# Performance work log

Measured on AMD Instinct MI355X. Metric: run time of the kernel, lower is better.

The kernel has to match this reference:

```python
import jax, jax.numpy as jnp
import numpy as np

RRF_K = 60.0
NUM_DOCS = 1_000_000


def setup_inputs() -> dict:
    key = jax.random.key(0)
    k1, k2, k3 = jax.random.split(key, 3)
    B, T, K = 60, 4, 100
    return {
        "index_tensor": jax.random.randint(k1, (B, T, K), 0, NUM_DOCS, dtype=jnp.int64 if jax.config.jax_enable_x64 else jnp.int32).astype(jnp.int32),
        "ranking_tensor": jax.random.uniform(k2, (B, T, K), dtype=jnp.float32),
        "weight": jnp.ones((T,), dtype=jnp.float32),
        "pos_positions": jax.random.randint(k3, (B,), 0, 5, dtype=jnp.int32),
        "num_docs": NUM_DOCS,
    }


def reference(index_tensor, ranking_tensor, weight, pos_positions, num_docs):
    # index_tensor: [B, T, K] doc ids; ranking_tensor: [B, T, K] teacher scores/ranks
    B = index_tensor.shape[0]
    # weighted reciprocal-rank-fusion score per retrieved doc: w_t / (RRF_K + rank)
    rrf = weight[None, :, None] / (RRF_K + ranking_tensor)  # [B, T, K]
    flat_idx = index_tensor.reshape(B, -1)                  # [B, T*K]
    flat_s = rrf.reshape(B, -1)                             # [B, T*K]
    # batched scatter-add into the per-query fused score vector [B, num_docs]
    fused = jnp.zeros((B, num_docs), dtype=ranking_tensor.dtype)
    fused = fused.at[jnp.arange(B)[:, None], flat_idx].add(flat_s)
    # full descending argsort per query (torch.argsort(..., descending=True))
    order = jnp.argsort(-fused, axis=1)                     # [B, num_docs]
    positive_idx = order[jnp.arange(B), pos_positions]      # [B]
    return order, positive_idx
```

## Files before the change

kernel.cpp:

```cpp
#include <hip/hip_runtime.h>
#include <hip/hip_bf16.h>

#define T_DIM 4
#define K_DIM 100
#define NPER 400
#define NDOCS 1000000
#define FILL_BLOCK 256
#define FILL_PER_THREAD 32
#define FILL_CHUNK (FILL_BLOCK * FILL_PER_THREAD)
#define BLOCKS_PER_ROW ((NDOCS + FILL_CHUNK - 1) / FILL_CHUNK)
#define QN (FILL_PER_THREAD / 4)

__global__ __launch_bounds__(512) void rrf_prep_kernel(
    const int* __restrict__ idx, const float* __restrict__ rnk,
    const float* __restrict__ weight, const int* __restrict__ pos,
    int* __restrict__ wsA, int* __restrict__ wsHead, int* __restrict__ wsNnz,
    int* __restrict__ out_pos)
{
  const int b = blockIdx.x;
  const int tid = threadIdx.x;
  const int lane = tid & 63, wave = tid >> 6;

  __shared__ int   ids[NPER];
  __shared__ float sc[NPER];
  __shared__ int   sid[NPER];
  __shared__ float ssc[NPER];
  __shared__ int   uid[NPER];
  __shared__ float usc[NPER];
  __shared__ int   head[NPER];
  __shared__ int   wsum[8];

  if (tid < NPER) {
    ids[tid] = idx[b * NPER + tid];
    sc[tid]  = weight[tid / K_DIM] / (60.0f + rnk[b * NPER + tid]);
  }
  __syncthreads();

  if (tid < NPER) {
    const int myid = ids[tid];
    int r = 0;
    for (int j = 0; j < NPER; ++j) {
      const int oj = ids[j];
      r += (oj < myid) || (oj == myid && j < tid);
    }
    sid[r] = myid;
    ssc[r] = sc[tid];
  }
  __syncthreads();

  int isLeader = 0;
  float mysum = 0.0f;
  if (tid < NPER) {
    isLeader = (tid == 0) || (sid[tid] != sid[tid - 1]);
    if (isLeader) {
      mysum = ssc[tid];
      for (int k = tid + 1; k < NPER && sid[k] == sid[tid]; ++k) mysum += ssc[k];
    }
  }

  int val = isLeader;
#pragma unroll
  for (int off = 1; off < 64; off <<= 1) {
    int n = __shfl_up(val, off, 64);
    if (lane >= off) val += n;
  }
  if (lane == 63) wsum[wave] = val;
  __syncthreads();
  if (wave == 0 && lane < 8) {
    int wv = wsum[lane];
#pragma unroll
    for (int off = 1; off < 8; off <<= 1) {
      int n = __shfl_up(wv, off, 8);
      if ((lane & 7) >= off) wv += n;
    }
    wsum[lane] = wv;
  }
  __syncthreads();
  const int incl = val + (wave > 0 ? wsum[wave - 1] : 0);
  const int nnz  = wsum[7];

  if (isLeader) {
    const int u = incl - 1;
    uid[u] = sid[tid];
    usc[u] = mysum;
  }
  __syncthreads();

  if (tid < nnz) {
    const float si = usc[tid];
    const int   ii = uid[tid];
    int r2 = 0;
    for (int j = 0; j < nnz; ++j) {
      const float sj = usc[j];
      r2 += (sj > si) || (sj == si && uid[j] < ii);
    }
    head[r2] = ii;
  }
  __syncthreads();

  if (tid < nnz) {
    wsA[b * NPER + tid]    = uid[tid] - tid;
    wsHead[b * NPER + tid] = head[tid];
  }
  if (tid == 0) {
    wsNnz[b]   = nnz;
    out_pos[b] = head[pos[b]];
  }
}

__global__ __launch_bounds__(FILL_BLOCK) void rrf_fill_kernel(
    const int* __restrict__ wsA, const int* __restrict__ wsHead,
    const int* __restrict__ wsNnz, int* __restrict__ out)
{
  const int row   = blockIdx.x / BLOCKS_PER_ROW;
  const int chunk = blockIdx.x % BLOCKS_PER_ROW;
  const int tid   = threadIdx.x;

  __shared__ int A[NPER];
  __shared__ int H[NPER];
  __shared__ int s_nnz;

  for (int i = tid; i < NPER; i += FILL_BLOCK)
    A[i] = wsA[row * NPER + i];
  if (chunk == 0)
    for (int i = tid; i < NPER; i += FILL_BLOCK)
      H[i] = wsHead[row * NPER + i];
  if (tid == 0) s_nnz = wsNnz[row];
  __syncthreads();
  const int nnz = s_nnz;

  const int chunkbase = chunk * FILL_CHUNK;
  int* outrow = out + (long long)row * NDOCS;

  if (chunkbase >= nnz && chunk + 1 < BLOCKS_PER_ROW) {
    const int z0   = chunkbase - nnz;
    const int zend = z0 + FILL_CHUNK - 1;

    int lo = 0, hi = nnz;
    while (lo < hi) { const int mid = (lo + hi) >> 1; if (A[mid] < z0) lo = mid + 1; else hi = mid; }
    const int j0 = lo;
    hi = nnz;
    while (lo < hi) { const int mid = (lo + hi) >> 1; if (A[mid] <= zend) lo = mid + 1; else hi = mid; }
    const int j1 = lo;

    const int za = z0 + tid * 4;
    int v[QN][4];
#pragma unroll
    for (int q = 0; q < QN; ++q) {
      const int b = za + q * 1024 + j0;
      v[q][0] = b; v[q][1] = b + 1; v[q][2] = b + 2; v[q][3] = b + 3;
    }
    for (int k = j0; k < j1; ++k) {
      const int a = A[k];
#pragma unroll
      for (int q = 0; q < QN; ++q) {
        const int z = za + q * 1024;
        v[q][0] += (a <= z);
        v[q][1] += (a <= z + 1);
        v[q][2] += (a <= z + 2);
        v[q][3] += (a <= z + 3);
      }
    }
#pragma unroll
    for (int q = 0; q < QN; ++q)
      *reinterpret_cast<int4*>(outrow + chunkbase + q * 1024 + tid * 4) =
          make_int4(v[q][0], v[q][1], v[q][2], v[q][3]);
  } else {
#pragma unroll
    for (int q = 0; q < QN; ++q) {
      const int p0 = chunkbase + q * 1024 + tid * 4;
      if (p0 >= NDOCS) continue;
      int vv[4];
#pragma unroll
      for (int k = 0; k < 4; ++k) {
        const int p = p0 + k;
        if (p < nnz) vv[k] = H[p];
        else {
          const int z = p - nnz;
          int lo = 0, hi = nnz;
          while (lo < hi) { const int mid = (lo + hi) >> 1; if (A[mid] <= z) lo = mid + 1; else hi = mid; }
          vv[k] = z + lo;
        }
      }
      *reinterpret_cast<int4*>(outrow + p0) = make_int4(vv[0], vv[1], vv[2], vv[3]);
    }
  }
}

extern "C" void kernel_launch(void* const* d_in, const int* in_sizes, int n_in,
                              void* d_out, int out_size, void* d_ws, size_t ws_size,
                              hipStream_t stream) {
  const int*   idx    = (const int*)d_in[0];
  const float* rnk    = (const float*)d_in[1];
  const float* weight = (const float*)d_in[2];
  const int*   pos    = (const int*)d_in[3];
  const int B = in_sizes[3];

  int* out = (int*)d_out;
  int* ws  = (int*)d_ws;
  int* wsA    = ws;
  int* wsHead = ws + (size_t)B * NPER;
  int* wsNnz  = ws + (size_t)2 * B * NPER;

  rrf_prep_kernel<<<B, 512, 0, stream>>>(idx, rnk, weight, pos,
                                         wsA, wsHead, wsNnz,
                                         out + (size_t)B * NDOCS);
  rrf_fill_kernel<<<B * BLOCKS_PER_ROW, FILL_BLOCK, 0, stream>>>(wsA, wsHead, wsNnz, out);
}
```

Before: 297.9 us.

## Precompute per-chunk breakpoint table in prep, halve fill chunk, vectorize rank loops

The prep kernel now writes a per-chunk table of the index ranges into the sorted nonzero offsets, so fill blocks skip their shared-memory staging, the barrier and both binary searches, and read the range endpoints directly from global memory. The per-thread fill work is halved, which doubles the number of fill blocks. The O(n^2) rank-counting loops in prep use vectorized int4/float4 LDS reads, with padding sentinels so the second loop runs a fixed trip count. In exchange there are more blocks to launch, and nonzero offsets are read from global/L2 inside the inner loop instead of from LDS. Only chunk 0 still stages data into shared memory.

```diff
diff --git a/kernel.cpp b/kernel.cpp
--- a/kernel.cpp
+++ b/kernel.cpp
@@ -6,28 +6,29 @@
 #define NPER 400
 #define NDOCS 1000000
 #define FILL_BLOCK 256
-#define FILL_PER_THREAD 32
+#define FILL_PER_THREAD 16
 #define FILL_CHUNK (FILL_BLOCK * FILL_PER_THREAD)
 #define BLOCKS_PER_ROW ((NDOCS + FILL_CHUNK - 1) / FILL_CHUNK)
 #define QN (FILL_PER_THREAD / 4)
+#define JTAB_W (BLOCKS_PER_ROW + 1)
 
 __global__ __launch_bounds__(512) void rrf_prep_kernel(
     const int* __restrict__ idx, const float* __restrict__ rnk,
     const float* __restrict__ weight, const int* __restrict__ pos,
     int* __restrict__ wsA, int* __restrict__ wsHead, int* __restrict__ wsNnz,
-    int* __restrict__ out_pos)
+    int* __restrict__ wsJ, int* __restrict__ out_pos)
 {
   const int b = blockIdx.x;
   const int tid = threadIdx.x;
   const int lane = tid & 63, wave = tid >> 6;
 
-  __shared__ int   ids[NPER];
-  __shared__ float sc[NPER];
-  __shared__ int   sid[NPER];
-  __shared__ float ssc[NPER];
-  __shared__ int   uid[NPER];
-  __shared__ float usc[NPER];
-  __shared__ int   head[NPER];
+  __shared__ alignas(16) int   ids[NPER];
+  __shared__ alignas(16) float sc[NPER];
+  __shared__ alignas(16) int   sid[NPER];
+  __shared__ alignas(16) float ssc[NPER];
+  __shared__ alignas(16) int   uid[NPER];
+  __shared__ alignas(16) float usc[NPER];
+  __shared__ alignas(16) int   head[NPER];
   __shared__ int   wsum[8];
 
   if (tid < NPER) {
@@ -39,9 +40,13 @@
   if (tid < NPER) {
     const int myid = ids[tid];
     int r = 0;
-    for (int j = 0; j < NPER; ++j) {
-      const int oj = ids[j];
-      r += (oj < myid) || (oj == myid && j < tid);
+#pragma unroll 4
+    for (int j4 = 0; j4 < NPER; j4 += 4) {
+      const int4 o = *reinterpret_cast<const int4*>(&ids[j4]);
+      r += (o.x < myid) || (o.x == myid && (j4 + 0) < tid);
+      r += (o.y < myid) || (o.y == myid && (j4 + 1) < tid);
+      r += (o.z < myid) || (o.z == myid && (j4 + 2) < tid);
+      r += (o.w < myid) || (o.w == myid && (j4 + 3) < tid);
     }
     sid[r] = myid;
     ssc[r] = sc[tid];
@@ -84,17 +89,33 @@
     uid[u] = sid[tid];
     usc[u] = mysum;
   }
+  if (tid >= nnz && tid < NPER) {
+    uid[tid] = 0x7fffffff;
+    usc[tid] = -1e30f;
+  }
   __syncthreads();
 
   if (tid < nnz) {
     const float si = usc[tid];
     const int   ii = uid[tid];
     int r2 = 0;
-    for (int j = 0; j < nnz; ++j) {
-      const float sj = usc[j];
-      r2 += (sj > si) || (sj == si && uid[j] < ii);
+#pragma unroll 4
+    for (int j4 = 0; j4 < NPER; j4 += 4) {
+      const float4 s4 = *reinterpret_cast<const float4*>(&usc[j4]);
+      const int4   u4 = *reinterpret_cast<const int4*>(&uid[j4]);
+      r2 += (s4.x > si) || (s4.x == si && u4.x < ii);
+      r2 += (s4.y > si) || (s4.y == si && u4.y < ii);
+      r2 += (s4.z > si) || (s4.z == si && u4.z < ii);
+      r2 += (s4.w > si) || (s4.w == si && u4.w < ii);
     }
     head[r2] = ii;
+  }
+
+  if (tid < JTAB_W) {
+    const int z0 = tid * FILL_CHUNK - nnz;
+    int lo = 0, hi = nnz;
+    while (lo < hi) { const int mid = (lo + hi) >> 1; if (uid[mid] - mid < z0) lo = mid + 1; else hi = mid; }
+    wsJ[b * JTAB_W + tid] = lo;
   }
   __syncthreads();
 
@@ -110,48 +131,34 @@
 
 __global__ __launch_bounds__(FILL_BLOCK) void rrf_fill_kernel(
     const int* __restrict__ wsA, const int* __restrict__ wsHead,
-    const int* __restrict__ wsNnz, int* __restrict__ out)
+    const int* __restrict__ wsNnz, const int* __restrict__ wsJ,
+    int* __restrict__ out)
 {
   const int row   = blockIdx.x / BLOCKS_PER_ROW;
   const int chunk = blockIdx.x % BLOCKS_PER_ROW;
   const int tid   = threadIdx.x;
+  const int chunkbase = chunk * FILL_CHUNK;
+  int* outrow = out + (long long)row * NDOCS;
 
   __shared__ int A[NPER];
   __shared__ int H[NPER];
-  __shared__ int s_nnz;
-
-  for (int i = tid; i < NPER; i += FILL_BLOCK)
-    A[i] = wsA[row * NPER + i];
-  if (chunk == 0)
-    for (int i = tid; i < NPER; i += FILL_BLOCK)
-      H[i] = wsHead[row * NPER + i];
-  if (tid == 0) s_nnz = wsNnz[row];
-  __syncthreads();
-  const int nnz = s_nnz;
-
-  const int chunkbase = chunk * FILL_CHUNK;
-  int* outrow = out + (long long)row * NDOCS;
-
-  if (chunkbase >= nnz && chunk + 1 < BLOCKS_PER_ROW) {
-    const int z0   = chunkbase - nnz;
-    const int zend = z0 + FILL_CHUNK - 1;
-
-    int lo = 0, hi = nnz;
-    while (lo < hi) { const int mid = (lo + hi) >> 1; if (A[mid] < z0) lo = mid + 1; else hi = mid; }
-    const int j0 = lo;
-    hi = nnz;
-    while (lo < hi) { const int mid = (lo + hi) >> 1; if (A[mid] <= zend) lo = mid + 1; else hi = mid; }
-    const int j1 = lo;
-
-    const int za = z0 + tid * 4;
+
+  if (chunk != 0) {
+    const int nnz = wsNnz[row];
+    const int j0  = wsJ[row * JTAB_W + chunk];
+    const int j1  = wsJ[row * JTAB_W + chunk + 1];
+    const int z0  = chunkbase - nnz;
+    const int za  = z0 + tid * 4;
+
     int v[QN][4];
 #pragma unroll
     for (int q = 0; q < QN; ++q) {
-      const int b = za + q * 1024 + j0;
-      v[q][0] = b; v[q][1] = b + 1; v[q][2] = b + 2; v[q][3] = b + 3;
-    }
+      const int bse = za + q * 1024 + j0;
+      v[q][0] = bse; v[q][1] = bse + 1; v[q][2] = bse + 2; v[q][3] = bse + 3;
+    }
+    const int* __restrict__ Arow = wsA + row * NPER;
     for (int k = j0; k < j1; ++k) {
-      const int a = A[k];
+      const int a = Arow[k];
 #pragma unroll
       for (int q = 0; q < QN; ++q) {
         const int z = za + q * 1024;
@@ -162,14 +169,25 @@
       }
     }
 #pragma unroll
-    for (int q = 0; q < QN; ++q)
-      *reinterpret_cast<int4*>(outrow + chunkbase + q * 1024 + tid * 4) =
-          make_int4(v[q][0], v[q][1], v[q][2], v[q][3]);
-  } else {
-#pragma unroll
     for (int q = 0; q < QN; ++q) {
       const int p0 = chunkbase + q * 1024 + tid * 4;
-      if (p0 >= NDOCS) continue;
+      if (p0 < NDOCS)
+        *reinterpret_cast<int4*>(outrow + p0) =
+            make_int4(v[q][0], v[q][1], v[q][2], v[q][3]);
+    }
+  } else {
+    __shared__ int s_nnz;
+    for (int i = tid; i < NPER; i += FILL_BLOCK) {
+      A[i] = wsA[row * NPER + i];
+      H[i] = wsHead[row * NPER + i];
+    }
+    if (tid == 0) s_nnz = wsNnz[row];
+    __syncthreads();
+    const int nnz = s_nnz;
+
+#pragma unroll
+    for (int q = 0; q < QN; ++q) {
+      const int p0 = q * 1024 + tid * 4;
       int vv[4];
 #pragma unroll
       for (int k = 0; k < 4; ++k) {
@@ -201,9 +219,10 @@
   int* wsA    = ws;
   int* wsHead = ws + (size_t)B * NPER;
   int* wsNnz  = ws + (size_t)2 * B * NPER;
+  int* wsJ    = wsNnz + B;
 
   rrf_prep_kernel<<<B, 512, 0, stream>>>(idx, rnk, weight, pos,
-                                         wsA, wsHead, wsNnz,
+                                         wsA, wsHead, wsNnz, wsJ,
                                          out + (size_t)B * NDOCS);
-  rrf_fill_kernel<<<B * BLOCKS_PER_ROW, FILL_BLOCK, 0, stream>>>(wsA, wsHead, wsNnz, out);
+  rrf_fill_kernel<<<B * BLOCKS_PER_ROW, FILL_BLOCK, 0, stream>>>(wsA, wsHead, wsNnz, wsJ, out);
 }
```

Result: faster. 270.7 us (-9.1%).
